# Kernel tuning notes

Hardware: AMD Instinct MI355X
Metric: run time of the kernel (lower is better)

Reference implementation:

```python
import jax, jax.numpy as jnp
import numpy as np

N_NODES = 100000
MAX_DEG = 16
D_IN = 256
D_OUT = 256


def setup_inputs() -> dict:
    key = jax.random.key(0)
    k1, k2, k3, k4, k5 = jax.random.split(key, 5)
    x = jax.random.normal(k1, (N_NODES, D_IN), dtype=jnp.float32)
    # padded edge list: -1 marks padding; first column always valid so degree >= 1
    col0 = jax.random.randint(k2, (N_NODES, 1), 0, N_NODES)
    rest = jax.random.randint(k3, (N_NODES, MAX_DEG - 1), -1, N_NODES)
    edge_index = jnp.concatenate([col0, rest], axis=1).astype(jnp.int64)
    # torch Linear(2*D_IN, D_OUT): weight [D_OUT, 2*D_IN], bias [D_OUT]
    W = jax.random.normal(k4, (D_OUT, 2 * D_IN), dtype=jnp.float32) * 0.05
    b = jax.random.normal(k5, (D_OUT,), dtype=jnp.float32) * 0.05
    return {"x": x, "edge_index": edge_index, "W": W, "b": b}


def reference(x, edge_index, W, b):
    # pad with a zero row so index -1 (padding) gathers zeros, matching torch
    padded = jnp.concatenate([x, jnp.zeros((1, x.shape[1]), dtype=x.dtype)], axis=0)
    neigh = padded[edge_index]  # [N, MAX_DEG, D_IN]
    degree = jnp.sum(edge_index >= 0, axis=-1, keepdims=True).astype(x.dtype)  # [N, 1]
    neigh_agg = jnp.sum(neigh, axis=1) / degree  # mean aggregation, [N, D_IN]
    h = jnp.concatenate([x, neigh_agg], axis=1)  # [N, 2*D_IN]
    return h @ W.T + b
```

## Files before the change

kernel.cpp:

```cpp
#include <hip/hip_runtime.h>
#include <stdint.h>


#define MAX_DEG 16
#define D_IN 256
#define D_OUT 256
#define N_NODES_C 100000
#define BM 64
#define LDS_A_STRIDE 264

typedef __attribute__((ext_vector_type(8))) short bf16x8;
typedef __attribute__((ext_vector_type(4))) float f32x4;

typedef const __attribute__((address_space(1))) void* gas_ptr;
typedef __attribute__((address_space(3))) void* las_ptr;

__device__ __forceinline__ uint32_t f2bf(float f) {
    union { float f; uint32_t u; } v; v.f = f;
    uint32_t u = v.u;
    return (u + 0x7FFFu + ((u >> 16) & 1u)) >> 16;
}
__device__ __forceinline__ uint32_t pack2(float lo, float hi) {
    return f2bf(lo) | (f2bf(hi) << 16);
}

__global__ __launch_bounds__(256) void cast_w2f_kernel(
    const float* __restrict__ W, ushort* __restrict__ Wb2f, ushort* __restrict__ y2)
{
    if (blockIdx.x < 64) {
        const int t = blockIdx.x * 256 + threadIdx.x;
        const int cg   = t >> 9;
        const int ks   = (t >> 6) & 7;
        const int lane = t & 63;
        const int quad = lane >> 4, r16 = lane & 15;
        const int c = cg * 16 + r16;
        const int k = ks * 32 + quad * 8;
        const float* src = W + (size_t)(c & 255) * 512 + (c >> 8) * 256 + k;
        float4 v0 = ((const float4*)src)[0];
        float4 v1 = ((const float4*)src)[1];
        uint4 p = { pack2(v0.x, v0.y), pack2(v0.z, v0.w),
                    pack2(v1.x, v1.y), pack2(v1.z, v1.w) };
        *(uint4*)(Wb2f + (size_t)t * 8) = p;
    } else {
        if (threadIdx.x < 32) {
            uint4 z = {0u, 0u, 0u, 0u};
            *(uint4*)(y2 + (size_t)N_NODES_C * 256 + threadIdx.x * 8) = z;
        }
    }
}

__global__ __launch_bounds__(512, 4) void gemm_xw_kernel(
    const float* __restrict__ x, const ushort* __restrict__ Wb2f,
    const float* __restrict__ bias, ushort* __restrict__ y2,
    float* __restrict__ out)
{
    __shared__ ushort sA[BM * LDS_A_STRIDE];

    const int tid = threadIdx.x;
    const int node0 = blockIdx.x * BM;

    {
        #pragma unroll
        for (int it = 0; it < 4; ++it) {
            const int idx = it * 512 + tid;
            const int row = idx >> 5;
            const int c8  = idx & 31;
            const int rg  = node0 + row;
            const float* src = x + (size_t)(rg < N_NODES_C ? rg : N_NODES_C - 1) * D_IN + c8 * 8;
            float4 v0 = ((const float4*)src)[0];
            float4 v1 = ((const float4*)src)[1];
            uint4 p = { pack2(v0.x, v0.y), pack2(v0.z, v0.w),
                        pack2(v1.x, v1.y), pack2(v1.z, v1.w) };
            *(uint4*)(sA + (size_t)row * LDS_A_STRIDE + c8 * 8) = p;
        }
    }
    __syncthreads();

    const int w = tid >> 6;
    const int lane = tid & 63;
    const int quad = lane >> 4;
    const int r16  = lane & 15;

    f32x4 acc[4][4];
    #pragma unroll
    for (int s = 0; s < 4; ++s)
        #pragma unroll
        for (int j = 0; j < 4; ++j)
            acc[s][j] = (f32x4){0.f, 0.f, 0.f, 0.f};

    const ushort* ap = sA + (size_t)r16 * LDS_A_STRIDE + quad * 8;
    const ushort* bp = Wb2f + ((size_t)(w * 4) * 8 + 0) * 64 * 8 + lane * 8;

    #pragma unroll
    for (int ks = 0; ks < D_IN / 32; ++ks) {
        bf16x8 a0 = *(const bf16x8*)(ap + 0  * 16 * LDS_A_STRIDE + ks * 32);
        bf16x8 a1 = *(const bf16x8*)(ap + 1  * 16 * LDS_A_STRIDE + ks * 32);
        bf16x8 a2 = *(const bf16x8*)(ap + 2  * 16 * LDS_A_STRIDE + ks * 32);
        bf16x8 a3 = *(const bf16x8*)(ap + 3  * 16 * LDS_A_STRIDE + ks * 32);
        #pragma unroll
        for (int j = 0; j < 4; ++j) {
            bf16x8 b = *(const bf16x8*)(bp + ((size_t)j * 8 + ks) * 64 * 8);
            acc[0][j] = __builtin_amdgcn_mfma_f32_16x16x32_bf16(a0, b, acc[0][j], 0, 0, 0);
            acc[1][j] = __builtin_amdgcn_mfma_f32_16x16x32_bf16(a1, b, acc[1][j], 0, 0, 0);
            acc[2][j] = __builtin_amdgcn_mfma_f32_16x16x32_bf16(a2, b, acc[2][j], 0, 0, 0);
            acc[3][j] = __builtin_amdgcn_mfma_f32_16x16x32_bf16(a3, b, acc[3][j], 0, 0, 0);
        }
    }

    if (w < 4) {
        #pragma unroll
        for (int j = 0; j < 4; ++j) {
            const int c = w * 64 + j * 16 + r16;
            const float bv = bias[c];
            #pragma unroll
            for (int s = 0; s < 4; ++s)
                #pragma unroll
                for (int r = 0; r < 4; ++r) {
                    const int row = node0 + s * 16 + quad * 4 + r;
                    if (row < N_NODES_C)
                        out[(size_t)row * D_OUT + c] = acc[s][j][r] + bv;
                }
        }
    } else {
        #pragma unroll
        for (int j = 0; j < 4; ++j) {
            const int c2 = (w - 4) * 64 + j * 16 + r16;
            #pragma unroll
            for (int s = 0; s < 4; ++s)
                #pragma unroll
                for (int r = 0; r < 4; ++r) {
                    const int row = node0 + s * 16 + quad * 4 + r;
                    if (row < N_NODES_C)
                        y2[(size_t)row * 256 + c2] = (ushort)f2bf(acc[s][j][r]);
                }
        }
    }
}

__global__ __launch_bounds__(256, 4) void gather_add_kernel(
    const ushort* __restrict__ y2, const int* __restrict__ edge,
    float* __restrict__ out)
{
    __shared__ char sBuf[4 * 8 * 1024];

    const int w4   = threadIdx.x >> 6;
    const int lane = threadIdx.x & 63;
    const int i = blockIdx.x * 4 + w4;

    const int e = edge[(size_t)i * MAX_DEG + (lane & 15)];
    const unsigned long long vm = __ballot(e >= 0);
    const int deg = (int)__popcll(vm & 0xFFFFull);
    const float inv = 1.0f / (float)deg;

    const uint32_t off_me = (uint32_t)(e < 0 ? N_NODES_C : e) * 512u;
    const char* yb = (const char*)y2;
    const uint32_t coff = (uint32_t)((lane & 31) * 16);

    const int cw = (lane & 31) * 8 + (lane >> 5) * 4;
    float* op = out + (size_t)i * D_OUT + cw;
    float4 yv = *(const float4*)op;

    char* lw = sBuf + (size_t)w4 * 8192;
    #pragma unroll
    for (int k = 0; k < 8; ++k) {
        const uint32_t ro = (uint32_t)__shfl((int)off_me, 2 * k + (lane >> 5), 64);
        const char* gsrc = yb + (size_t)(ro + coff);
        __builtin_amdgcn_global_load_lds((gas_ptr)gsrc, (las_ptr)(lw + k * 1024),
                                         16, 0, 0);
    }
    asm volatile("s_waitcnt vmcnt(0)" ::: "memory");
    __builtin_amdgcn_sched_barrier(0);

    float a[8];
    #pragma unroll
    for (int q = 0; q < 8; ++q) a[q] = 0.f;
    #pragma unroll
    for (int k = 0; k < 8; ++k) {
        uint4 g = *(const uint4*)(lw + k * 1024 + lane * 16);
        uint32_t u[4] = { g.x, g.y, g.z, g.w };
        #pragma unroll
        for (int q = 0; q < 4; ++q) {
            union { uint32_t ui; float f; } lo, hi;
            lo.ui = u[q] << 16;
            hi.ui = u[q] & 0xFFFF0000u;
            a[2*q]   += lo.f;
            a[2*q+1] += hi.f;
        }
    }
    #pragma unroll
    for (int q = 0; q < 8; ++q) a[q] += __shfl_xor(a[q], 32, 64);

    const int q0 = (lane >> 5) * 4;
    float4 r;
    r.x = yv.x + inv * a[q0 + 0];
    r.y = yv.y + inv * a[q0 + 1];
    r.z = yv.z + inv * a[q0 + 2];
    r.w = yv.w + inv * a[q0 + 3];
    *(float4*)op = r;
}

#define D_K 512
#define LDS_STRIDE 520

__global__ __launch_bounds__(256) void cast_w_kernel(const float* __restrict__ W,
                                                     ushort* __restrict__ Wb) {
    int i = (blockIdx.x * 256 + threadIdx.x) * 4;
    float4 v = *(const float4*)(W + i);
    ushort4 p = { (ushort)f2bf(v.x), (ushort)f2bf(v.y),
                  (ushort)f2bf(v.z), (ushort)f2bf(v.w) };
    *(ushort4*)(Wb + i) = p;
}

__global__ __launch_bounds__(256) void sage_fp32_kernel(
    const float* __restrict__ x, const int* __restrict__ edge,
    const ushort* __restrict__ Wb, const float* __restrict__ bias,
    float* __restrict__ out)
{
    __shared__ ushort sH[32 * LDS_STRIDE];
    const int tid = threadIdx.x;
    const int node0 = blockIdx.x * 32;
    {
        const int m = tid >> 3, l = tid & 7;
        const int node = node0 + m;
        const float4* xrow = (const float4*)(x + (size_t)node * D_IN);
        ushort* dst = sH + m * LDS_STRIDE + l * 32;
        #pragma unroll
        for (int q = 0; q < 8; ++q) {
            float4 v = xrow[l * 8 + q];
            ushort4 p = { (ushort)f2bf(v.x), (ushort)f2bf(v.y),
                          (ushort)f2bf(v.z), (ushort)f2bf(v.w) };
            *(ushort4*)(dst + q * 4) = p;
        }
        float4 agg[8];
        #pragma unroll
        for (int q = 0; q < 8; ++q) agg[q] = make_float4(0.f,0.f,0.f,0.f);
        int deg = 0;
        for (int d = 0; d < MAX_DEG; ++d) {
            int nb = edge[(size_t)node * MAX_DEG + d];
            if (nb >= 0) {
                ++deg;
                const float4* nr = (const float4*)(x + (size_t)nb * D_IN);
                #pragma unroll
                for (int q = 0; q < 8; ++q) {
                    float4 t = nr[l * 8 + q];
                    agg[q].x += t.x; agg[q].y += t.y;
                    agg[q].z += t.z; agg[q].w += t.w;
                }
            }
        }
        const float inv = 1.0f / (float)deg;
        ushort* dst2 = sH + m * LDS_STRIDE + D_IN + l * 32;
        #pragma unroll
        for (int q = 0; q < 8; ++q) {
            ushort4 p = { (ushort)f2bf(agg[q].x*inv), (ushort)f2bf(agg[q].y*inv),
                          (ushort)f2bf(agg[q].z*inv), (ushort)f2bf(agg[q].w*inv) };
            *(ushort4*)(dst2 + q * 4) = p;
        }
    }
    __syncthreads();
    {
        const int wave = tid >> 6, lane = tid & 63;
        const int quad = lane >> 4, r16 = lane & 15;
        const int mt = wave & 1, nh = wave >> 1;
        f32x4 acc[8];
        #pragma unroll
        for (int j = 0; j < 8; ++j) {
            float bv = bias[(nh * 8 + j) * 16 + r16];
            acc[j] = (f32x4){bv, bv, bv, bv};
        }
        const ushort* arow = sH + (mt * 16 + r16) * LDS_STRIDE + quad * 8;
        #pragma unroll
        for (int ks = 0; ks < D_K / 32; ++ks) {
            bf16x8 a = *(const bf16x8*)(arow + ks * 32);
            #pragma unroll
            for (int j = 0; j < 8; ++j) {
                const int o = (nh * 8 + j) * 16 + r16;
                bf16x8 b = *(const bf16x8*)(Wb + (size_t)o * D_K + ks * 32 + quad * 8);
                acc[j] = __builtin_amdgcn_mfma_f32_16x16x32_bf16(a, b, acc[j], 0, 0, 0);
            }
        }
        #pragma unroll
        for (int j = 0; j < 8; ++j) {
            const int o = (nh * 8 + j) * 16 + r16;
            #pragma unroll
            for (int r = 0; r < 4; ++r) {
                const int row = node0 + mt * 16 + quad * 4 + r;
                out[(size_t)row * D_OUT + o] = acc[j][r];
            }
        }
    }
}

extern "C" void kernel_launch(void* const* d_in, const int* in_sizes, int n_in,
                              void* d_out, int out_size, void* d_ws, size_t ws_size,
                              hipStream_t stream) {
    const float* x    = (const float*)d_in[0];
    const int*   edge = (const int*)d_in[1];
    const float* W    = (const float*)d_in[2];
    const float* bias = (const float*)d_in[3];
    float* out = (float*)d_out;

    const size_t y2_bytes = (size_t)(N_NODES_C + 1) * 256 * 2;
    const size_t wb_bytes = (size_t)512 * 256 * 2;
    const int n = in_sizes[0] / D_IN;

    if (ws_size >= y2_bytes + wb_bytes) {
        ushort* y2   = (ushort*)d_ws;
        ushort* Wb2f = (ushort*)((char*)d_ws + y2_bytes);
        cast_w2f_kernel<<<65, 256, 0, stream>>>(W, Wb2f, y2);
        gemm_xw_kernel<<<(n + BM - 1) / BM, 512, 0, stream>>>(x, Wb2f, bias, y2, out);
        gather_add_kernel<<<n / 4, 256, 0, stream>>>(y2, edge, out);
    } else {
        ushort* Wb = (ushort*)d_ws;
        cast_w_kernel<<<(D_OUT * D_K) / 1024, 256, 0, stream>>>(W, Wb);
        sage_fp32_kernel<<<n / 32, 256, 0, stream>>>(x, edge, Wb, bias, out);
    }
}
```

Before: 376.6 us.

## Make gather kernel persistent per wave with double-buffered LDS prefetch

The gather-add kernel is restructured so each wave handles 16 consecutive nodes instead of one. While it accumulates the current node it prefetches the next node's neighbour rows into a second LDS buffer using global_load_lds, and loads edge indices two nodes ahead. This is meant to hide gather latency and cut per-node launch and setup cost. In exchange it needs a hand-tuned vmcnt wait count and launches fewer, smaller blocks, which may lower parallelism across the GPU.

After: 384.4 us. 2.1% more time.

```diff
diff --git a/kernel.cpp b/kernel.cpp
--- a/kernel.cpp
+++ b/kernel.cpp
@@ -8,6 +8,7 @@
 #define N_NODES_C 100000
 #define BM 64
 #define LDS_A_STRIDE 264
+#define NPW 16
 
 typedef __attribute__((ext_vector_type(8))) short bf16x8;
 typedef __attribute__((ext_vector_type(4))) float f32x4;
@@ -137,66 +138,90 @@
     }
 }
 
-__global__ __launch_bounds__(256, 4) void gather_add_kernel(
+__global__ __launch_bounds__(128) void gather_add_kernel(
     const ushort* __restrict__ y2, const int* __restrict__ edge,
     float* __restrict__ out)
 {
-    __shared__ char sBuf[4 * 8 * 1024];
-
-    const int w4   = threadIdx.x >> 6;
+    __shared__ char sBuf[2 * 2 * 8192];
+
+    const int wv   = threadIdx.x >> 6;
     const int lane = threadIdx.x & 63;
-    const int i = blockIdx.x * 4 + w4;
-
-    const int e = edge[(size_t)i * MAX_DEG + (lane & 15)];
-    const unsigned long long vm = __ballot(e >= 0);
-    const int deg = (int)__popcll(vm & 0xFFFFull);
-    const float inv = 1.0f / (float)deg;
-
-    const uint32_t off_me = (uint32_t)(e < 0 ? N_NODES_C : e) * 512u;
+    const int gw   = blockIdx.x * 2 + wv;
+    const int base = gw * NPW;
+    if (base >= N_NODES_C) return;
+    const int count = min(NPW, N_NODES_C - base);
+
+    char* bc = sBuf + wv * 16384;
+    char* bn = bc + 8192;
+
     const char* yb = (const char*)y2;
     const uint32_t coff = (uint32_t)((lane & 31) * 16);
-
-    const int cw = (lane & 31) * 8 + (lane >> 5) * 4;
-    float* op = out + (size_t)i * D_OUT + cw;
-    float4 yv = *(const float4*)op;
-
-    char* lw = sBuf + (size_t)w4 * 8192;
-    #pragma unroll
-    for (int k = 0; k < 8; ++k) {
-        const uint32_t ro = (uint32_t)__shfl((int)off_me, 2 * k + (lane >> 5), 64);
-        const char* gsrc = yb + (size_t)(ro + coff);
-        __builtin_amdgcn_global_load_lds((gas_ptr)gsrc, (las_ptr)(lw + k * 1024),
-                                         16, 0, 0);
-    }
-    asm volatile("s_waitcnt vmcnt(0)" ::: "memory");
-    __builtin_amdgcn_sched_barrier(0);
-
-    float a[8];
-    #pragma unroll
-    for (int q = 0; q < 8; ++q) a[q] = 0.f;
-    #pragma unroll
-    for (int k = 0; k < 8; ++k) {
-        uint4 g = *(const uint4*)(lw + k * 1024 + lane * 16);
-        uint32_t u[4] = { g.x, g.y, g.z, g.w };
-        #pragma unroll
-        for (int q = 0; q < 4; ++q) {
-            union { uint32_t ui; float f; } lo, hi;
-            lo.ui = u[q] << 16;
-            hi.ui = u[q] & 0xFFFF0000u;
-            a[2*q]   += lo.f;
-            a[2*q+1] += hi.f;
-        }
-    }
-    #pragma unroll
-    for (int q = 0; q < 8; ++q) a[q] += __shfl_xor(a[q], 32, 64);
-
-    const int q0 = (lane >> 5) * 4;
-    float4 r;
-    r.x = yv.x + inv * a[q0 + 0];
-    r.y = yv.y + inv * a[q0 + 1];
-    r.z = yv.z + inv * a[q0 + 2];
-    r.w = yv.w + inv * a[q0 + 3];
-    *(float4*)op = r;
+    const int l15  = lane & 15;
+    const int half = lane >> 5;
+    const int cw   = (lane & 31) * 8 + half * 4;
+
+    int ecur = edge[(size_t)base * MAX_DEG + l15];
+    const int t1p = (1 < count) ? 1 : count - 1;
+    int enxt = edge[(size_t)(base + t1p) * MAX_DEG + l15];
+    float4 yvcur = *(const float4*)(out + (size_t)base * D_OUT + cw);
+    {
+        const uint32_t om = (uint32_t)(ecur < 0 ? N_NODES_C : ecur) * 512u;
+        #pragma unroll
+        for (int k = 0; k < 8; ++k) {
+            const uint32_t ro = (uint32_t)__shfl((int)om, 2 * k + half, 64);
+            __builtin_amdgcn_global_load_lds((gas_ptr)(yb + (size_t)(ro + coff)),
+                                             (las_ptr)(bc + k * 1024), 16, 0, 0);
+        }
+    }
+
+    for (int t = 0; t < count; ++t) {
+        const int t2 = (t + 2 < count) ? t + 2 : count - 1;
+        const int e2 = edge[(size_t)(base + t2) * MAX_DEG + l15];
+        {
+            const uint32_t om = (uint32_t)(enxt < 0 ? N_NODES_C : enxt) * 512u;
+            #pragma unroll
+            for (int k = 0; k < 8; ++k) {
+                const uint32_t ro = (uint32_t)__shfl((int)om, 2 * k + half, 64);
+                __builtin_amdgcn_global_load_lds((gas_ptr)(yb + (size_t)(ro + coff)),
+                                                 (las_ptr)(bn + k * 1024), 16, 0, 0);
+            }
+        }
+        const int t1 = (t + 1 < count) ? t + 1 : count - 1;
+        float4 yvn = *(const float4*)(out + (size_t)(base + t1) * D_OUT + cw);
+        asm volatile("s_waitcnt vmcnt(11)" ::: "memory");
+        __builtin_amdgcn_sched_barrier(0);
+        const int deg = (int)__popcll(__ballot(ecur >= 0) & 0xFFFFull);
+        const float inv = 1.0f / (float)deg;
+        float a[8];
+        #pragma unroll
+        for (int q = 0; q < 8; ++q) a[q] = 0.f;
+        #pragma unroll
+        for (int k = 0; k < 8; ++k) {
+            uint4 g = *(const uint4*)(bc + k * 1024 + lane * 16);
+            uint32_t u[4] = { g.x, g.y, g.z, g.w };
+            #pragma unroll
+            for (int q = 0; q < 4; ++q) {
+                union { uint32_t ui; float f; } lo, hi;
+                lo.ui = u[q] << 16;
+                hi.ui = u[q] & 0xFFFF0000u;
+                a[2*q]   += lo.f;
+                a[2*q+1] += hi.f;
+            }
+        }
+        #pragma unroll
+        for (int q = 0; q < 8; ++q) a[q] += __shfl_xor(a[q], 32, 64);
+
+        const int q0 = half * 4;
+        float4 r;
+        r.x = yvcur.x + inv * a[q0 + 0];
+        r.y = yvcur.y + inv * a[q0 + 1];
+        r.z = yvcur.z + inv * a[q0 + 2];
+        r.w = yvcur.w + inv * a[q0 + 3];
+        *(float4*)(out + (size_t)(base + t) * D_OUT + cw) = r;
+
+        ecur = enxt; enxt = e2; yvcur = yvn;
+        char* tmp = bc; bc = bn; bn = tmp;
+    }
 }
 
 #define D_K 512
@@ -309,7 +334,8 @@
         ushort* Wb2f = (ushort*)((char*)d_ws + y2_bytes);
         cast_w2f_kernel<<<65, 256, 0, stream>>>(W, Wb2f, y2);
         gemm_xw_kernel<<<(n + BM - 1) / BM, 512, 0, stream>>>(x, Wb2f, bias, y2, out);
-        gather_add_kernel<<<n / 4, 256, 0, stream>>>(y2, edge, out);
+        const int nwaves = (n + NPW - 1) / NPW;
+        gather_add_kernel<<<(nwaves + 1) / 2, 128, 0, stream>>>(y2, edge, out);
     } else {
         ushort* Wb = (ushort*)d_ws;
         cast_w_kernel<<<(D_OUT * D_K) / 1024, 256, 0, stream>>>(W, Wb);
```

## Stage x via direct global-to-LDS loads and store intermediate output as bf16

Applied to the files above, without the earlier changes.

The GEMM kernel now copies fp32 x rows straight into LDS with async global_load_lds using an XOR swizzle, and converts them to bf16 while building the MFMA fragments, instead of converting in registers before the LDS write. The x@W1+b partial result is written as bf16 into the first half of each output row, halving that intermediate write and the gather kernel's read of it. The gather kernel's occupancy hint rises from 4 to 5. The cost is twice the LDS footprint in the GEMM, conversion work repeated per wave, and extra bf16 rounding of the self term, which may hurt accuracy.

Result: no change. 373.7 us (-0.8%).

```diff
diff --git a/kernel.cpp b/kernel.cpp
--- a/kernel.cpp
+++ b/kernel.cpp
@@ -7,7 +7,6 @@
 #define D_OUT 256
 #define N_NODES_C 100000
 #define BM 64
-#define LDS_A_STRIDE 264
 
 typedef __attribute__((ext_vector_type(8))) short bf16x8;
 typedef __attribute__((ext_vector_type(4))) float f32x4;
@@ -54,32 +53,27 @@
     const float* __restrict__ bias, ushort* __restrict__ y2,
     float* __restrict__ out)
 {
-    __shared__ ushort sA[BM * LDS_A_STRIDE];
+    __shared__ float sX[BM * 256];
 
     const int tid = threadIdx.x;
     const int node0 = blockIdx.x * BM;
-
-    {
-        #pragma unroll
-        for (int it = 0; it < 4; ++it) {
-            const int idx = it * 512 + tid;
-            const int row = idx >> 5;
-            const int c8  = idx & 31;
-            const int rg  = node0 + row;
-            const float* src = x + (size_t)(rg < N_NODES_C ? rg : N_NODES_C - 1) * D_IN + c8 * 8;
-            float4 v0 = ((const float4*)src)[0];
-            float4 v1 = ((const float4*)src)[1];
-            uint4 p = { pack2(v0.x, v0.y), pack2(v0.z, v0.w),
-                        pack2(v1.x, v1.y), pack2(v1.z, v1.w) };
-            *(uint4*)(sA + (size_t)row * LDS_A_STRIDE + c8 * 8) = p;
-        }
-    }
-    __syncthreads();
-
     const int w = tid >> 6;
     const int lane = tid & 63;
+
+    #pragma unroll
+    for (int it = 0; it < 8; ++it) {
+        const int R = w * 8 + it;
+        const int rg = node0 + R;
+        const float* rowp = x + (size_t)(rg < N_NODES_C ? rg : N_NODES_C - 1) * D_IN;
+        const char* gsrc = (const char*)rowp + ((lane ^ it) << 4);
+        __builtin_amdgcn_global_load_lds((gas_ptr)gsrc,
+            (las_ptr)((char*)sX + (size_t)R * 1024), 16, 0, 0);
+    }
+    __syncthreads();
+
     const int quad = lane >> 4;
     const int r16  = lane & 15;
+    const int x7   = r16 & 7;
 
     f32x4 acc[4][4];
     #pragma unroll
@@ -88,22 +82,34 @@
         for (int j = 0; j < 4; ++j)
             acc[s][j] = (f32x4){0.f, 0.f, 0.f, 0.f};
 
-    const ushort* ap = sA + (size_t)r16 * LDS_A_STRIDE + quad * 8;
+    const char* aB[4];
+    #pragma unroll
+    for (int s = 0; s < 4; ++s)
+        aB[s] = (const char*)sX + (size_t)(s * 16 + r16) * 1024;
     const ushort* bp = Wb2f + ((size_t)(w * 4) * 8 + 0) * 64 * 8 + lane * 8;
 
     #pragma unroll
     for (int ks = 0; ks < D_IN / 32; ++ks) {
-        bf16x8 a0 = *(const bf16x8*)(ap + 0  * 16 * LDS_A_STRIDE + ks * 32);
-        bf16x8 a1 = *(const bf16x8*)(ap + 1  * 16 * LDS_A_STRIDE + ks * 32);
-        bf16x8 a2 = *(const bf16x8*)(ap + 2  * 16 * LDS_A_STRIDE + ks * 32);
-        bf16x8 a3 = *(const bf16x8*)(ap + 3  * 16 * LDS_A_STRIDE + ks * 32);
+        const int ch = ks * 8 + quad * 2;
+        bf16x8 afr[4];
+        #pragma unroll
+        for (int s = 0; s < 4; ++s) {
+            f32x4 lo = *(const f32x4*)(aB[s] + ((ch ^ x7) << 4));
+            f32x4 hi = *(const f32x4*)(aB[s] + (((ch + 1) ^ x7) << 4));
+            union { uint32_t u[4]; bf16x8 v; } cv;
+            cv.u[0] = pack2(lo.x, lo.y);
+            cv.u[1] = pack2(lo.z, lo.w);
+            cv.u[2] = pack2(hi.x, hi.y);
+            cv.u[3] = pack2(hi.z, hi.w);
+            afr[s] = cv.v;
+        }
         #pragma unroll
         for (int j = 0; j < 4; ++j) {
             bf16x8 b = *(const bf16x8*)(bp + ((size_t)j * 8 + ks) * 64 * 8);
-            acc[0][j] = __builtin_amdgcn_mfma_f32_16x16x32_bf16(a0, b, acc[0][j], 0, 0, 0);
-            acc[1][j] = __builtin_amdgcn_mfma_f32_16x16x32_bf16(a1, b, acc[1][j], 0, 0, 0);
-            acc[2][j] = __builtin_amdgcn_mfma_f32_16x16x32_bf16(a2, b, acc[2][j], 0, 0, 0);
-            acc[3][j] = __builtin_amdgcn_mfma_f32_16x16x32_bf16(a3, b, acc[3][j], 0, 0, 0);
+            acc[0][j] = __builtin_amdgcn_mfma_f32_16x16x32_bf16(afr[0], b, acc[0][j], 0, 0, 0);
+            acc[1][j] = __builtin_amdgcn_mfma_f32_16x16x32_bf16(afr[1], b, acc[1][j], 0, 0, 0);
+            acc[2][j] = __builtin_amdgcn_mfma_f32_16x16x32_bf16(afr[2], b, acc[2][j], 0, 0, 0);
+            acc[3][j] = __builtin_amdgcn_mfma_f32_16x16x32_bf16(afr[3], b, acc[3][j], 0, 0, 0);
         }
     }
 
@@ -118,7 +124,8 @@
                 for (int r = 0; r < 4; ++r) {
                     const int row = node0 + s * 16 + quad * 4 + r;
                     if (row < N_NODES_C)
-                        out[(size_t)row * D_OUT + c] = acc[s][j][r] + bv;
+                        ((ushort*)(out + (size_t)row * D_OUT))[c] =
+                            (ushort)f2bf(acc[s][j][r] + bv);
                 }
         }
     } else {
@@ -137,7 +144,7 @@
     }
 }
 
-__global__ __launch_bounds__(256, 4) void gather_add_kernel(
+__global__ __launch_bounds__(256, 5) void gather_add_kernel(
     const ushort* __restrict__ y2, const int* __restrict__ edge,
     float* __restrict__ out)
 {
@@ -155,15 +162,16 @@
     const uint32_t off_me = (uint32_t)(e < 0 ? N_NODES_C : e) * 512u;
     const char* yb = (const char*)y2;
     const uint32_t coff = (uint32_t)((lane & 31) * 16);
-
-    const int cw = (lane & 31) * 8 + (lane >> 5) * 4;
+    const int half = lane >> 5;
+
+    const int cw = (lane & 31) * 8 + half * 4;
     float* op = out + (size_t)i * D_OUT + cw;
-    float4 yv = *(const float4*)op;
+    const uint2 y1p = *(const uint2*)((const char*)(out + (size_t)i * D_OUT) + cw * 2);
 
     char* lw = sBuf + (size_t)w4 * 8192;
     #pragma unroll
     for (int k = 0; k < 8; ++k) {
-        const uint32_t ro = (uint32_t)__shfl((int)off_me, 2 * k + (lane >> 5), 64);
+        const uint32_t ro = (uint32_t)__shfl((int)off_me, 2 * k + half, 64);
         const char* gsrc = yb + (size_t)(ro + coff);
         __builtin_amdgcn_global_load_lds((gas_ptr)gsrc, (las_ptr)(lw + k * 1024),
                                          16, 0, 0);
@@ -190,12 +198,15 @@
     #pragma unroll
     for (int q = 0; q < 8; ++q) a[q] += __shfl_xor(a[q], 32, 64);
 
-    const int q0 = (lane >> 5) * 4;
+    const int q0 = half * 4;
+    union { uint32_t ui; float f; } c0, c1, c2, c3;
+    c0.ui = y1p.x << 16; c1.ui = y1p.x & 0xFFFF0000u;
+    c2.ui = y1p.y << 16; c3.ui = y1p.y & 0xFFFF0000u;
     float4 r;
-    r.x = yv.x + inv * a[q0 + 0];
-    r.y = yv.y + inv * a[q0 + 1];
-    r.z = yv.z + inv * a[q0 + 2];
-    r.w = yv.w + inv * a[q0 + 3];
+    r.x = c0.f + inv * a[q0 + 0];
+    r.y = c1.f + inv * a[q0 + 1];
+    r.z = c2.f + inv * a[q0 + 2];
+    r.w = c3.f + inv * a[q0 + 3];
     *(float4*)op = r;
 }
 
```
